# Performance work log

Measured on AMD Instinct MI355X. Metric: run time of the kernel, lower is better.

The kernel has to match this reference:

```python
import jax, jax.numpy as jnp
import numpy as np

LN_EPS = 1e-12  # BERT default layer_norm_eps


def setup_inputs() -> dict:
    key = jax.random.key(0)
    ks = jax.random.split(key, 8)
    B, S, H, I, E = 4, 2048, 1024, 4096, 8
    sH = 1.0 / np.sqrt(H)
    sI = 1.0 / np.sqrt(I)
    return {
        "hidden_states": jax.random.normal(ks[0], (B, S, H), dtype=jnp.float32),
        "Wr": jax.random.uniform(ks[1], (E, H), jnp.float32, -sH, sH),      # router (no bias)
        "W1": jax.random.uniform(ks[2], (E, H, I), jnp.float32, -sH, sH),   # per-expert BertIntermediate
        "b1": jax.random.uniform(ks[3], (E, I), jnp.float32, -sH, sH),
        "Wo": jax.random.uniform(ks[4], (I, H), jnp.float32, -sI, sI),      # shared BertOutput dense
        "bo": jax.random.uniform(ks[5], (H,), jnp.float32, -sI, sI),
        "gamma": jnp.ones((H,), jnp.float32),
        "beta": jnp.zeros((H,), jnp.float32),
    }


def reference(hidden_states, Wr, W1, b1, Wo, bo, gamma, beta):
    B, S, H = hidden_states.shape
    E = Wr.shape[0]
    x = hidden_states.reshape(-1, H)                      # [N, H]
    router_logits = x @ Wr.T                              # [N, E]
    # top-1 expert per token (router probs are NOT used to scale outputs in the original)
    expert_idx = jnp.argmax(jax.nn.softmax(router_logits, axis=-1), axis=-1)  # [N]
    # dispatch == per-token expert FFN; accumulate masked per-expert outputs
    inter = jnp.zeros((x.shape[0], W1.shape[2]), dtype=x.dtype)  # [N, I]
    for e in range(E):  # fixed small expert count
        mask = (expert_idx == e)[:, None].astype(x.dtype)
        inter = inter + mask * jax.nn.gelu(x @ W1[e] + b1[e], approximate=False)
    # shared BertOutput: dense -> (dropout off) -> residual -> LayerNorm
    y = inter @ Wo + bo + x                               # [N, H]
    mu = jnp.mean(y, axis=-1, keepdims=True)
    var = jnp.mean(jnp.square(y - mu), axis=-1, keepdims=True)
    out = (y - mu) * jax.lax.rsqrt(var + LN_EPS) * gamma + beta
    return out.reshape(B, S, H)
```

## Files before the change

### kernel.cpp

```cpp
#include <hip/hip_runtime.h>
#include <hip/hip_bf16.h>
#include <math.h>

#define NTOK 8192
#define HD 1024
#define ID 4096
#define NE 8
#define MAXTILES 72
#define SORTT 512
#define TPT (NTOK / SORTT)

typedef __attribute__((ext_vector_type(8))) short short8;
typedef __attribute__((ext_vector_type(8))) unsigned short ushort8;
typedef __attribute__((ext_vector_type(4))) float floatx4;

__device__ __forceinline__ unsigned short f2bf(float f) {
  unsigned int u = __float_as_uint(f);
  return (unsigned short)((u + 0x7fffu + ((u >> 16) & 1u)) >> 16);
}

__device__ __forceinline__ void async_ld16(const void* g, void* l) {
  __builtin_amdgcn_global_load_lds(
      (const __attribute__((address_space(1))) unsigned int*)g,
      (__attribute__((address_space(3))) unsigned int*)l,
      16, 0, 0);
}


__device__ __forceinline__ void transpose_tile256(const float* __restrict__ src,
                                                  unsigned short* __restrict__ dst,
                                                  int R, int C, int bx, int by, int bz,
                                                  unsigned short (*t)[72]) {
  size_t bo = (size_t)bz * R * C;
  src += bo; dst += bo;
  int c0 = bx * 64, r0 = by * 256;
  int tid = threadIdx.x;
  int rr = tid >> 4, cc = tid & 15;
#pragma unroll
  for (int p = 0; p < 16; p++) {
    int r = p * 16 + rr;
    float4 v = *(const float4*)(src + (size_t)(r0 + r) * C + c0 + cc * 4);
    int gs = cc ^ ((r >> 3) & 15);
    ushort4 o;
    o.x = f2bf(v.x); o.y = f2bf(v.y); o.z = f2bf(v.z); o.w = f2bf(v.w);
    *(ushort4*)&t[r][gs * 4] = o;
  }
  __syncthreads();
  int rc = tid & 31;
  int cb = tid >> 5;
#pragma unroll
  for (int p = 0; p < 8; p++) {
    int c = p * 8 + cb;
    int col = ((c >> 2) ^ (rc & 15)) * 4 + (c & 3);
    ushort8 o;
#pragma unroll
    for (int i = 0; i < 8; i++) o[i] = t[rc * 8 + i][col];
    *(ushort8*)(dst + (size_t)(c0 + c) * R + r0 + rc * 8) = o;
  }
}

__device__ __forceinline__ void router_body(const float* __restrict__ x,
                                            const float* __restrict__ wr,
                                            int* __restrict__ eidx,
                                            unsigned short* __restrict__ xb, int nbase) {
  int wave = threadIdx.x >> 6, lane = threadIdx.x & 63;
  int n = nbase + wave;
  const float* xr = x + (size_t)n * HD;
  unsigned short* xbr = xb + (size_t)n * HD;
  double acc[NE];
#pragma unroll
  for (int e = 0; e < NE; e++) acc[e] = 0.0;
#pragma unroll
  for (int v = 0; v < 4; v++) {
    int h = (lane + v * 64) * 4;
    float4 xv = *(const float4*)(xr + h);
    ushort4 o;
    o.x = f2bf(xv.x); o.y = f2bf(xv.y); o.z = f2bf(xv.z); o.w = f2bf(xv.w);
    *(ushort4*)(xbr + h) = o;
#pragma unroll
    for (int e = 0; e < NE; e++) {
      float4 wv = *(const float4*)(wr + e * HD + h);
      acc[e] += (double)xv.x * wv.x + (double)xv.y * wv.y +
                (double)xv.z * wv.z + (double)xv.w * wv.w;
    }
  }
#pragma unroll
  for (int m = 32; m >= 1; m >>= 1) {
#pragma unroll
    for (int e = 0; e < NE; e++) acc[e] += __shfl_xor(acc[e], m, 64);
  }
  if (lane == 0) {
    int best = 0; double bv = acc[0];
#pragma unroll
    for (int e = 1; e < NE; e++) if (acc[e] > bv) { bv = acc[e]; best = e; }
    eidx[n] = best;
  }
}

__global__ void preamble_kernel(const float* __restrict__ x, const float* __restrict__ wr,
                                const float* __restrict__ w1, const float* __restrict__ wo,
                                unsigned short* __restrict__ w1t, unsigned short* __restrict__ wot,
                                int* __restrict__ eidx, unsigned short* __restrict__ xb) {
  __shared__ unsigned short tile[256][72];
  int b = blockIdx.x;
  if (b < 2048) {
    int e = b >> 8, rem = b & 255;
    transpose_tile256(w1, w1t, HD, ID, rem & 63, rem >> 6, e, tile);
  } else if (b < 2304) {
    int bb = b - 2048;
    transpose_tile256(wo, wot, ID, HD, bb & 15, bb >> 4, 0, tile);
  } else {
    router_body(x, wr, eidx, xb, (b - 2304) * 4);
  }
}

__global__ __launch_bounds__(SORTT) void sort_kernel(
    const int* __restrict__ eidx, int* __restrict__ ntiles, int* __restrict__ tile_e,
    int* __restrict__ tile_base, int* __restrict__ tile_len, int* __restrict__ perm) {
  __shared__ int h[NE][SORTT];
  __shared__ int off_sh[NE];
  __shared__ int tot[NE];
  int t = threadIdx.x;
  int wave = t >> 6, lane = t & 63;
  const int base = t * TPT;

  int4 e0 = *(const int4*)(eidx + base);
  int4 e1 = *(const int4*)(eidx + base + 4);
  int4 e2 = *(const int4*)(eidx + base + 8);
  int4 e3 = *(const int4*)(eidx + base + 12);
  int ex[TPT] = {e0.x, e0.y, e0.z, e0.w, e1.x, e1.y, e1.z, e1.w,
                 e2.x, e2.y, e2.z, e2.w, e3.x, e3.y, e3.z, e3.w};
  int cnt0 = 0, cnt1 = 0, cnt2 = 0, cnt3 = 0, cnt4 = 0, cnt5 = 0, cnt6 = 0, cnt7 = 0;
#pragma unroll
  for (int i = 0; i < TPT; i++) {
    int e = ex[i];
    cnt0 += (e == 0); cnt1 += (e == 1); cnt2 += (e == 2); cnt3 += (e == 3);
    cnt4 += (e == 4); cnt5 += (e == 5); cnt6 += (e == 6); cnt7 += (e == 7);
  }
  h[0][t] = cnt0; h[1][t] = cnt1; h[2][t] = cnt2; h[3][t] = cnt3;
  h[4][t] = cnt4; h[5][t] = cnt5; h[6][t] = cnt6; h[7][t] = cnt7;
  __syncthreads();

  {
    int e = wave;
    int v[8], s = 0;
#pragma unroll
    for (int i = 0; i < 8; i++) { v[i] = h[e][lane * 8 + i]; s += v[i]; }
    int inc = s;
#pragma unroll
    for (int d = 1; d < 64; d <<= 1) {
      int o = __shfl_up(inc, d, 64);
      if (lane >= d) inc += o;
    }
    int exc = inc - s;
#pragma unroll
    for (int i = 0; i < 8; i++) { h[e][lane * 8 + i] = exc; exc += v[i]; }
    if (lane == 63) tot[e] = inc;
  }
  __syncthreads();

  if (t == 0) {
    int s = 0, tt = 0;
    for (int e = 0; e < NE; e++) {
      off_sh[e] = s;
      int c = tot[e];
      for (int b = 0; b < c; b += 128) {
        tile_e[tt] = e;
        tile_base[tt] = s + b;
        tile_len[tt] = (c - b < 128) ? (c - b) : 128;
        tt++;
      }
      s += c;
    }
    *ntiles = tt;
  }
  __syncthreads();

  int c0c = off_sh[0] + h[0][t], c1c = off_sh[1] + h[1][t];
  int c2c = off_sh[2] + h[2][t], c3c = off_sh[3] + h[3][t];
  int c4c = off_sh[4] + h[4][t], c5c = off_sh[5] + h[5][t];
  int c6c = off_sh[6] + h[6][t], c7c = off_sh[7] + h[7][t];
#pragma unroll
  for (int i = 0; i < TPT; i++) {
    int e = ex[i];
    int pos = c0c;
    pos = (e == 1) ? c1c : pos; pos = (e == 2) ? c2c : pos;
    pos = (e == 3) ? c3c : pos; pos = (e == 4) ? c4c : pos;
    pos = (e == 5) ? c5c : pos; pos = (e == 6) ? c6c : pos;
    pos = (e == 7) ? c7c : pos;
    perm[pos] = base + i;
    c0c += (e == 0); c1c += (e == 1); c2c += (e == 2); c3c += (e == 3);
    c4c += (e == 4); c5c += (e == 5); c6c += (e == 6); c7c += (e == 7);
  }
}


__global__ __launch_bounds__(256, 2) void ffn1_kernel(
    const unsigned short* __restrict__ xb, const unsigned short* __restrict__ w1t,
    const float* __restrict__ b1, const int* __restrict__ perm,
    const int* __restrict__ ntiles, const int* __restrict__ tile_e,
    const int* __restrict__ tile_base, const int* __restrict__ tile_len,
    unsigned short* __restrict__ interb) {
  int w = blockIdx.x;
  int x = w & 7, s = w >> 3;
  int nq = x & 3, th = x >> 2;
  int t = th * 36 + (s >> 3);
  if (t >= *ntiles) return;
  int nb = (nq * 8 + (s & 7)) * 128;
  int e = tile_e[t], base = tile_base[t], len = tile_len[t];

  __shared__ unsigned short lA[128 * 64];
  __shared__ unsigned short lB[128 * 64];

  int tid = threadIdx.x;
  int wave = tid >> 6, lane = tid & 63;
  int lr = lane >> 3;
  int chunk = (lane & 7) ^ lr;

  const unsigned short* gA[4];
  const unsigned short* gB[4];
#pragma unroll
  for (int qq = 0; qq < 4; qq++) {
    int c = wave * 4 + qq;
    int tr = c * 8 + lr;
    int token = perm[base + (tr < len ? tr : len - 1)];
    gA[qq] = xb + (size_t)token * HD + chunk * 8;
    int nr = nb + c * 8 + lr;
    gB[qq] = w1t + ((size_t)e * ID + nr) * HD + chunk * 8;
  }

  floatx4 acc[4][4];
#pragma unroll
  for (int i = 0; i < 4; i++)
#pragma unroll
    for (int j = 0; j < 4; j++) acc[i][j] = (floatx4){0.f, 0.f, 0.f, 0.f};

  int wm = (wave >> 1) * 64, wn = (wave & 1) * 64;
  int c15 = lane & 15, q4 = lane >> 4;

  for (int ko = 0; ko < HD / 64; ko++) {
#pragma unroll
    for (int qq = 0; qq < 4; qq++) {
      int c = wave * 4 + qq;
      async_ld16(gA[qq] + ko * 64, &lA[c * 512]);
      async_ld16(gB[qq] + ko * 64, &lB[c * 512]);
    }
    __syncthreads();
#pragma unroll
    for (int kk = 0; kk < 2; kk++) {
      short8 af[4], bfr[4];
#pragma unroll
      for (int i = 0; i < 4; i++) {
        int m = wm + i * 16 + c15;
        int sa = (kk * 4 + q4) ^ (m & 7);
        af[i] = *(const short8*)&lA[m * 64 + sa * 8];
        int n = wn + i * 16 + c15;
        int sb = (kk * 4 + q4) ^ (n & 7);
        bfr[i] = *(const short8*)&lB[n * 64 + sb * 8];
      }
#pragma unroll
      for (int i = 0; i < 4; i++)
#pragma unroll
        for (int j = 0; j < 4; j++)
          acc[i][j] = __builtin_amdgcn_mfma_f32_16x16x32_bf16(af[i], bfr[j], acc[i][j], 0, 0, 0);
    }
    __syncthreads();
  }

#pragma unroll
  for (int i = 0; i < 4; i++) {
#pragma unroll
    for (int r = 0; r < 4; r++) {
      int tr = wm + i * 16 + q4 * 4 + r;
      if (tr >= len) continue;
      int token = perm[base + tr];
#pragma unroll
      for (int j = 0; j < 4; j++) {
        int col = nb + wn + j * 16 + c15;
        float v = acc[i][j][r] + b1[e * ID + col];
        v = 0.5f * v * (1.0f + erff(v * 0.70710678118654752f));
        interb[(size_t)token * ID + col] = f2bf(v);
      }
    }
  }
}

__global__ __launch_bounds__(256, 2) void ffn2_kernel(
    const unsigned short* __restrict__ interb, const unsigned short* __restrict__ wot,
    const float* __restrict__ bo, const float* __restrict__ x, float* __restrict__ y) {
  int w = blockIdx.x;
  int x8 = w & 7, s = w >> 3;
  int nq = x8 & 3, mh = x8 >> 2;
  int tm = mh * 32 + (s >> 1);
  int nb = (nq * 2 + (s & 1)) * 128;

  __shared__ unsigned short lA[128 * 64];
  __shared__ unsigned short lB[128 * 64];

  int tid = threadIdx.x;
  int wave = tid >> 6, lane = tid & 63;
  int lr = lane >> 3;
  int chunk = (lane & 7) ^ lr;

  const unsigned short* gA[4];
  const unsigned short* gB[4];
#pragma unroll
  for (int qq = 0; qq < 4; qq++) {
    int c = wave * 4 + qq;
    int row = tm * 128 + c * 8 + lr;
    gA[qq] = interb + (size_t)row * ID + chunk * 8;
    int nr = nb + c * 8 + lr;
    gB[qq] = wot + (size_t)nr * ID + chunk * 8;
  }

  floatx4 acc[4][4];
#pragma unroll
  for (int i = 0; i < 4; i++)
#pragma unroll
    for (int j = 0; j < 4; j++) acc[i][j] = (floatx4){0.f, 0.f, 0.f, 0.f};

  int wm = (wave >> 1) * 64, wn = (wave & 1) * 64;
  int c15 = lane & 15, q4 = lane >> 4;

  for (int ko = 0; ko < ID / 64; ko++) {
#pragma unroll
    for (int qq = 0; qq < 4; qq++) {
      int c = wave * 4 + qq;
      async_ld16(gA[qq] + ko * 64, &lA[c * 512]);
      async_ld16(gB[qq] + ko * 64, &lB[c * 512]);
    }
    __syncthreads();
#pragma unroll
    for (int kk = 0; kk < 2; kk++) {
      short8 af[4], bfr[4];
#pragma unroll
      for (int i = 0; i < 4; i++) {
        int m = wm + i * 16 + c15;
        int sa = (kk * 4 + q4) ^ (m & 7);
        af[i] = *(const short8*)&lA[m * 64 + sa * 8];
        int n = wn + i * 16 + c15;
        int sb = (kk * 4 + q4) ^ (n & 7);
        bfr[i] = *(const short8*)&lB[n * 64 + sb * 8];
      }
#pragma unroll
      for (int i = 0; i < 4; i++)
#pragma unroll
        for (int j = 0; j < 4; j++)
          acc[i][j] = __builtin_amdgcn_mfma_f32_16x16x32_bf16(af[i], bfr[j], acc[i][j], 0, 0, 0);
    }
    __syncthreads();
  }

#pragma unroll
  for (int i = 0; i < 4; i++) {
#pragma unroll
    for (int r = 0; r < 4; r++) {
      int row = tm * 128 + wm + i * 16 + q4 * 4 + r;
#pragma unroll
      for (int j = 0; j < 4; j++) {
        int col = nb + wn + j * 16 + c15;
        float v = acc[i][j][r] + bo[col] + x[(size_t)row * HD + col];
        y[(size_t)row * HD + col] = v;
      }
    }
  }
}

__global__ void ln_kernel(float* __restrict__ y, const float* __restrict__ gamma,
                          const float* __restrict__ beta) {
  int row = blockIdx.x, t = threadIdx.x;
  int lane = t & 63, wave = t >> 6;
  float* yr = y + (size_t)row * HD;
  float4 v = *(const float4*)(yr + t * 4);
  float s = v.x + v.y + v.z + v.w;
  float ss = v.x * v.x + v.y * v.y + v.z * v.z + v.w * v.w;
#pragma unroll
  for (int m = 32; m >= 1; m >>= 1) {
    s += __shfl_xor(s, m, 64);
    ss += __shfl_xor(ss, m, 64);
  }
  __shared__ float sred[4], ssred[4];
  if (lane == 0) { sred[wave] = s; ssred[wave] = ss; }
  __syncthreads();
  s = sred[0] + sred[1] + sred[2] + sred[3];
  ss = ssred[0] + ssred[1] + ssred[2] + ssred[3];
  float mu = s * (1.0f / HD);
  float var = ss * (1.0f / HD) - mu * mu;
  float rs = rsqrtf(var + 1e-12f);
  float4 g = *(const float4*)(gamma + t * 4);
  float4 b = *(const float4*)(beta + t * 4);
  float4 o;
  o.x = (v.x - mu) * rs * g.x + b.x;
  o.y = (v.y - mu) * rs * g.y + b.y;
  o.z = (v.z - mu) * rs * g.z + b.z;
  o.w = (v.w - mu) * rs * g.w + b.w;
  *(float4*)(yr + t * 4) = o;
}


extern "C" void kernel_launch(void* const* d_in, const int* in_sizes, int n_in,
                              void* d_out, int out_size, void* d_ws, size_t ws_size,
                              hipStream_t stream) {
  const float* x     = (const float*)d_in[0];
  const float* wr    = (const float*)d_in[1];
  const float* w1    = (const float*)d_in[2];
  const float* b1    = (const float*)d_in[3];
  const float* wo    = (const float*)d_in[4];
  const float* bo    = (const float*)d_in[5];
  const float* gamma = (const float*)d_in[6];
  const float* beta  = (const float*)d_in[7];
  float* out = (float*)d_out;

  char* p = (char*)d_ws;
  unsigned short* w1t = (unsigned short*)p; p += (size_t)NE * ID * HD * 2;
  unsigned short* wot = (unsigned short*)p; p += (size_t)HD * ID * 2;
  unsigned short* xb  = (unsigned short*)p; p += (size_t)NTOK * HD * 2;
  unsigned short* interb = (unsigned short*)p; p += (size_t)NTOK * ID * 2;
  int* eidx = (int*)p; p += (size_t)NTOK * 4;
  int* perm = (int*)p; p += (size_t)NTOK * 4;
  int* ints = (int*)p;
  int* ntiles    = ints;
  int* tile_e    = ints + 8;
  int* tile_base = ints + 80;
  int* tile_len  = ints + 152;

  preamble_kernel<<<4352, 256, 0, stream>>>(x, wr, w1, wo, w1t, wot, eidx, xb);
  sort_kernel<<<1, SORTT, 0, stream>>>(eidx, ntiles, tile_e, tile_base, tile_len, perm);
  ffn1_kernel<<<2304, 256, 0, stream>>>(
      xb, w1t, b1, perm, ntiles, tile_e, tile_base, tile_len, interb);
  ffn2_kernel<<<512, 256, 0, stream>>>(interb, wot, bo, x, out);
  ln_kernel<<<NTOK, 256, 0, stream>>>(out, gamma, beta);
}
```

Baseline: 468.7 us.

## Split router into own kernel and merge sort with weight transposes

Router and bf16 conversion of x now run in a separate kernel first. The single-block sort is folded into the weight-transpose kernel as block 0, so it runs alongside the transposes instead of as its own serial one-block launch. Transpose blocks move to 512 threads, with each thread doing half as many loads and stores. The cost is one extra launch boundary before the transposes and a larger block size for the transpose work.

```diff
diff --git a/kernel.cpp b/kernel.cpp
--- a/kernel.cpp
+++ b/kernel.cpp
@@ -27,44 +27,10 @@
 }
 
 
-__device__ __forceinline__ void transpose_tile256(const float* __restrict__ src,
-                                                  unsigned short* __restrict__ dst,
-                                                  int R, int C, int bx, int by, int bz,
-                                                  unsigned short (*t)[72]) {
-  size_t bo = (size_t)bz * R * C;
-  src += bo; dst += bo;
-  int c0 = bx * 64, r0 = by * 256;
-  int tid = threadIdx.x;
-  int rr = tid >> 4, cc = tid & 15;
-#pragma unroll
-  for (int p = 0; p < 16; p++) {
-    int r = p * 16 + rr;
-    float4 v = *(const float4*)(src + (size_t)(r0 + r) * C + c0 + cc * 4);
-    int gs = cc ^ ((r >> 3) & 15);
-    ushort4 o;
-    o.x = f2bf(v.x); o.y = f2bf(v.y); o.z = f2bf(v.z); o.w = f2bf(v.w);
-    *(ushort4*)&t[r][gs * 4] = o;
-  }
-  __syncthreads();
-  int rc = tid & 31;
-  int cb = tid >> 5;
-#pragma unroll
-  for (int p = 0; p < 8; p++) {
-    int c = p * 8 + cb;
-    int col = ((c >> 2) ^ (rc & 15)) * 4 + (c & 3);
-    ushort8 o;
-#pragma unroll
-    for (int i = 0; i < 8; i++) o[i] = t[rc * 8 + i][col];
-    *(ushort8*)(dst + (size_t)(c0 + c) * R + r0 + rc * 8) = o;
-  }
-}
-
-__device__ __forceinline__ void router_body(const float* __restrict__ x,
-                                            const float* __restrict__ wr,
-                                            int* __restrict__ eidx,
-                                            unsigned short* __restrict__ xb, int nbase) {
+__global__ void router_kernel(const float* __restrict__ x, const float* __restrict__ wr,
+                              int* __restrict__ eidx, unsigned short* __restrict__ xb) {
   int wave = threadIdx.x >> 6, lane = threadIdx.x & 63;
-  int n = nbase + wave;
+  int n = blockIdx.x * 4 + wave;
   const float* xr = x + (size_t)n * HD;
   unsigned short* xbr = xb + (size_t)n * HD;
   double acc[NE];
@@ -97,29 +63,46 @@
   }
 }
 
-__global__ void preamble_kernel(const float* __restrict__ x, const float* __restrict__ wr,
-                                const float* __restrict__ w1, const float* __restrict__ wo,
-                                unsigned short* __restrict__ w1t, unsigned short* __restrict__ wot,
-                                int* __restrict__ eidx, unsigned short* __restrict__ xb) {
-  __shared__ unsigned short tile[256][72];
-  int b = blockIdx.x;
-  if (b < 2048) {
-    int e = b >> 8, rem = b & 255;
-    transpose_tile256(w1, w1t, HD, ID, rem & 63, rem >> 6, e, tile);
-  } else if (b < 2304) {
-    int bb = b - 2048;
-    transpose_tile256(wo, wot, ID, HD, bb & 15, bb >> 4, 0, tile);
-  } else {
-    router_body(x, wr, eidx, xb, (b - 2304) * 4);
-  }
-}
-
-__global__ __launch_bounds__(SORTT) void sort_kernel(
-    const int* __restrict__ eidx, int* __restrict__ ntiles, int* __restrict__ tile_e,
-    int* __restrict__ tile_base, int* __restrict__ tile_len, int* __restrict__ perm) {
-  __shared__ int h[NE][SORTT];
-  __shared__ int off_sh[NE];
-  __shared__ int tot[NE];
+
+__device__ __forceinline__ void transpose_tile256_512(const float* __restrict__ src,
+                                                      unsigned short* __restrict__ dst,
+                                                      int R, int C, int bx, int by, int bz,
+                                                      unsigned short (*t)[72]) {
+  size_t bo = (size_t)bz * R * C;
+  src += bo; dst += bo;
+  int c0 = bx * 64, r0 = by * 256;
+  int tid = threadIdx.x;
+  int rr = tid >> 4, cc = tid & 15;
+#pragma unroll
+  for (int p = 0; p < 8; p++) {
+    int r = p * 32 + rr;
+    float4 v = *(const float4*)(src + (size_t)(r0 + r) * C + c0 + cc * 4);
+    int gs = cc ^ ((r >> 3) & 15);
+    ushort4 o;
+    o.x = f2bf(v.x); o.y = f2bf(v.y); o.z = f2bf(v.z); o.w = f2bf(v.w);
+    *(ushort4*)&t[r][gs * 4] = o;
+  }
+  __syncthreads();
+  int rc = tid & 31;
+  int cb = tid >> 5;
+#pragma unroll
+  for (int p = 0; p < 4; p++) {
+    int c = p * 16 + cb;
+    int col = ((c >> 2) ^ (rc & 15)) * 4 + (c & 3);
+    ushort8 o;
+#pragma unroll
+    for (int i = 0; i < 8; i++) o[i] = t[rc * 8 + i][col];
+    *(ushort8*)(dst + (size_t)(c0 + c) * R + r0 + rc * 8) = o;
+  }
+}
+
+__device__ __forceinline__ void sort_body(const int* __restrict__ eidx, int* __restrict__ ntiles,
+                                          int* __restrict__ tile_e, int* __restrict__ tile_base,
+                                          int* __restrict__ tile_len, int* __restrict__ perm,
+                                          char* smem) {
+  int (*h)[SORTT] = (int(*)[SORTT])smem;
+  int* off_sh = (int*)(smem + NE * SORTT * 4);
+  int* tot = off_sh + NE;
   int t = threadIdx.x;
   int wave = t >> 6, lane = t & 63;
   const int base = t * TPT;
@@ -191,6 +174,27 @@
     perm[pos] = base + i;
     c0c += (e == 0); c1c += (e == 1); c2c += (e == 2); c3c += (e == 3);
     c4c += (e == 4); c5c += (e == 5); c6c += (e == 6); c7c += (e == 7);
+  }
+}
+
+__global__ __launch_bounds__(512) void tsort_kernel(
+    const float* __restrict__ w1, const float* __restrict__ wo,
+    unsigned short* __restrict__ w1t, unsigned short* __restrict__ wot,
+    const int* __restrict__ eidx, int* __restrict__ ntiles, int* __restrict__ tile_e,
+    int* __restrict__ tile_base, int* __restrict__ tile_len, int* __restrict__ perm) {
+  __shared__ char smem[256 * 72 * 2];
+  int b = blockIdx.x;
+  if (b == 0) {
+    sort_body(eidx, ntiles, tile_e, tile_base, tile_len, perm, smem);
+  } else if (b < 2049) {
+    int bb = b - 1;
+    int e = bb >> 8, rem = bb & 255;
+    transpose_tile256_512(w1, w1t, HD, ID, rem & 63, rem >> 6, e,
+                          (unsigned short(*)[72])smem);
+  } else {
+    int bb = b - 2049;
+    transpose_tile256_512(wo, wot, ID, HD, bb & 15, bb >> 4, 0,
+                          (unsigned short(*)[72])smem);
   }
 }
 
@@ -424,8 +428,9 @@
   int* tile_base = ints + 80;
   int* tile_len  = ints + 152;
 
-  preamble_kernel<<<4352, 256, 0, stream>>>(x, wr, w1, wo, w1t, wot, eidx, xb);
-  sort_kernel<<<1, SORTT, 0, stream>>>(eidx, ntiles, tile_e, tile_base, tile_len, perm);
+  router_kernel<<<NTOK / 4, 256, 0, stream>>>(x, wr, eidx, xb);
+  tsort_kernel<<<2305, 512, 0, stream>>>(w1, wo, w1t, wot, eidx, ntiles,
+                                         tile_e, tile_base, tile_len, perm);
   ffn1_kernel<<<2304, 256, 0, stream>>>(
       xb, w1t, b1, perm, ntiles, tile_e, tile_base, tile_len, interb);
   ffn2_kernel<<<512, 256, 0, stream>>>(interb, wot, bo, x, out);
```

New measurement: 488.1 us. 4.1% more time.
